# Optimization experiments

Hardware: AMD Instinct MI355X
Metric: run time of the kernel (lower is better)

The kernel has to match this reference:

```python
import jax, jax.numpy as jnp
import numpy as np

EMBED = 1024
HEADS = 16
HEAD_DIM = EMBED // HEADS


def setup_inputs() -> dict:
    key = jax.random.key(0)
    ks = jax.random.split(key, 9)
    N, S = 2, 2048
    values = jax.random.normal(ks[0], (N, S, EMBED), dtype=jnp.float32)
    keys = jax.random.normal(ks[1], (N, S, EMBED), dtype=jnp.float32)
    queries = jax.random.normal(ks[2], (N, S, EMBED), dtype=jnp.float32)
    mask = jax.random.randint(ks[3], (N, 1, S, S), 0, 2, dtype=jnp.int32)
    sc_h = 1.0 / np.sqrt(HEAD_DIM)
    sc_e = 1.0 / np.sqrt(EMBED)
    Wv = jax.random.normal(ks[4], (HEAD_DIM, HEAD_DIM), dtype=jnp.float32) * sc_h
    Wk = jax.random.normal(ks[5], (HEAD_DIM, HEAD_DIM), dtype=jnp.float32) * sc_h
    Wq = jax.random.normal(ks[6], (HEAD_DIM, HEAD_DIM), dtype=jnp.float32) * sc_h
    Wo = jax.random.normal(ks[7], (EMBED, EMBED), dtype=jnp.float32) * sc_e
    bo = jax.random.normal(ks[8], (EMBED,), dtype=jnp.float32) * 0.01
    return {"values": values, "keys": keys, "queries": queries, "mask": mask,
            "Wv": Wv, "Wk": Wk, "Wq": Wq, "Wo": Wo, "bo": bo}


def reference(values, keys, queries, mask, Wv, Wk, Wq, Wo, bo):
    N, S, _ = queries.shape
    H, D = HEADS, HEAD_DIM
    # split heads: [N, S, H, D]
    v = values.reshape(N, -1, H, D) @ Wv.T
    k = keys.reshape(N, -1, H, D) @ Wk.T
    q = queries.reshape(N, -1, H, D) @ Wq.T
    # [N, H, Q, K] scores
    energy = jnp.einsum('nqhd,nkhd->nhqk', q, k)
    energy = jnp.where(mask == 0, jnp.float32(1e-12), energy)
    attention = jax.nn.softmax(energy / np.sqrt(D), axis=3)
    # faithful to source einsum 'NVHD,NHQK->NQHD' (sums V and K independently)
    out = jnp.einsum('nvhd,nhqk->nqhd', v, attention).reshape(N, S, H * D)
    return out @ Wo.T + bo
```

## Files before the change

kernel.cpp:

```cpp
#include <hip/hip_runtime.h>

#define NB     2
#define SEQ    2048
#define EMBED  1024
#define HEADS  16
#define HDIM   64
#define CH     128
#define ROWS   (SEQ / CH)

__global__ __launch_bounds__(256) void colsum_part(const float* __restrict__ vals,
                                                   float* __restrict__ part) {
    const int b = blockIdx.x;
    const int n = b >> 7;
    const int c = b & 127;
    const int t = threadIdx.x;
    const float4* base = reinterpret_cast<const float4*>(vals)
                       + (size_t)(n * SEQ + c * ROWS) * (EMBED / 4);
    float4 acc = make_float4(0.f, 0.f, 0.f, 0.f);
    #pragma unroll 8
    for (int r = 0; r < ROWS; ++r) {
        float4 v = base[(size_t)r * (EMBED / 4) + t];
        acc.x += v.x; acc.y += v.y; acc.z += v.z; acc.w += v.w;
    }
    reinterpret_cast<float4*>(part)[(size_t)b * (EMBED / 4) + t] = acc;
}

__global__ __launch_bounds__(256) void mv_bcast(const float* __restrict__ part,
                                                const float* __restrict__ Wv,
                                                const float* __restrict__ Wo,
                                                const float* __restrict__ bo,
                                                float4* __restrict__ out4) {
    const int b   = blockIdx.x;
    const int wn  = b >> 6;
    const int s16 = b & 63;
    const int t   = threadIdx.x;
    __shared__ float svl[EMBED];
    __shared__ float vfl[EMBED];
    __shared__ float rsl[16];

    {
        const float4* p = reinterpret_cast<const float4*>(part)
                        + (size_t)wn * CH * (EMBED / 4) + t;
        float4 acc = make_float4(0.f, 0.f, 0.f, 0.f);
        #pragma unroll 8
        for (int c = 0; c < CH; ++c) {
            float4 v = p[(size_t)c * (EMBED / 4)];
            acc.x += v.x; acc.y += v.y; acc.z += v.z; acc.w += v.w;
        }
        reinterpret_cast<float4*>(svl)[t] = acc;
    }
    __syncthreads();

    for (int o = t; o < EMBED; o += 256) {
        const int h = o >> 6, d = o & 63;
        const float* wr = Wv + d * HDIM;
        const float* sr = svl + h * HDIM;
        float a = 0.f;
        #pragma unroll
        for (int e = 0; e < HDIM; ++e) a += wr[e] * sr[e];
        vfl[o] = a;
    }
    __syncthreads();

    const int wave = t >> 6;
    const int lane = t & 63;
    float4 vv[4];
    #pragma unroll
    for (int it = 0; it < 4; ++it)
        vv[it] = reinterpret_cast<const float4*>(vfl)[it * 64 + lane];

    const float4* Wo4 = reinterpret_cast<const float4*>(Wo);
    #pragma unroll
    for (int j = 0; j < 4; ++j) {
        const int o = s16 * 16 + wave * 4 + j;
        float acc = 0.f;
        #pragma unroll
        for (int it = 0; it < 4; ++it) {
            float4 w4 = Wo4[(size_t)o * (EMBED / 4) + it * 64 + lane];
            acc += w4.x * vv[it].x + w4.y * vv[it].y
                 + w4.z * vv[it].z + w4.w * vv[it].w;
        }
        #pragma unroll
        for (int off = 32; off >= 1; off >>= 1)
            acc += __shfl_xor(acc, off);
        if (lane == 0) rsl[wave * 4 + j] = acc + bo[o];
    }
    __syncthreads();

    const float4 val = reinterpret_cast<const float4*>(rsl)[t & 3];
    float4* o = out4 + (size_t)wn * SEQ * (EMBED / 4) + (s16 * 4 + (t & 3))
              + (size_t)(t >> 2) * (EMBED / 4);
    #pragma unroll 8
    for (int k = 0; k < 32; ++k)
        o[(size_t)k * 64 * (EMBED / 4)] = val;
}

extern "C" void kernel_launch(void* const* d_in, const int* in_sizes, int n_in,
                              void* d_out, int out_size, void* d_ws, size_t ws_size,
                              hipStream_t stream) {
    const float* vals = (const float*)d_in[0];
    const float* Wv   = (const float*)d_in[4];
    const float* Wo   = (const float*)d_in[7];
    const float* bo   = (const float*)d_in[8];
    float* out = (float*)d_out;

    float* part = (float*)d_ws;

    colsum_part<<<NB * CH, 256, 0, stream>>>(vals, part);
    mv_bcast<<<NB * 64, 256, 0, stream>>>(part, Wv, Wo, bo, (float4*)out);
}
```

Measured before the change: 136.4 us.

## Fuse column-sum and matvec-broadcast into one kernel with global flag sync

Merges the two launches into a single 256-block kernel. Each block first writes its partial column sums and sets a flag. Designated blocks wait on those flags, reduce the partials and publish them with a second set of flags. Every block then waits for the reduced sums and runs the matvec and broadcast. This removes one kernel launch and the gap between the two kernels. In exchange it relies on all blocks being resident at once, and the flags keep the same magic value and are never reset, so on repeated calls the waits may pass early and read stale data.

Result: slower. 169.8 us (+24.5%).

```diff
diff --git a/kernel.cpp b/kernel.cpp
--- a/kernel.cpp
+++ b/kernel.cpp
@@ -3,52 +3,75 @@
 #define NB     2
 #define SEQ    2048
 #define EMBED  1024
-#define HEADS  16
 #define HDIM   64
-#define CH     128
-#define ROWS   (SEQ / CH)
+#define MAGIC  0x3C3C3C3Cu
 
-__global__ __launch_bounds__(256) void colsum_part(const float* __restrict__ vals,
-                                                   float* __restrict__ part) {
+__global__ __launch_bounds__(256) void fused_k(
+    const float* __restrict__ vals, const float* __restrict__ Wv,
+    const float* __restrict__ Wo,  const float* __restrict__ bo,
+    float* __restrict__ part, float* __restrict__ Sv,
+    unsigned* __restrict__ flag1, unsigned* __restrict__ flag2,
+    float4* __restrict__ out4)
+{
     const int b = blockIdx.x;
     const int n = b >> 7;
-    const int c = b & 127;
+    const int j = b & 127;
     const int t = threadIdx.x;
-    const float4* base = reinterpret_cast<const float4*>(vals)
-                       + (size_t)(n * SEQ + c * ROWS) * (EMBED / 4);
-    float4 acc = make_float4(0.f, 0.f, 0.f, 0.f);
-    #pragma unroll 8
-    for (int r = 0; r < ROWS; ++r) {
-        float4 v = base[(size_t)r * (EMBED / 4) + t];
-        acc.x += v.x; acc.y += v.y; acc.z += v.z; acc.w += v.w;
-    }
-    reinterpret_cast<float4*>(part)[(size_t)b * (EMBED / 4) + t] = acc;
-}
 
-__global__ __launch_bounds__(256) void mv_bcast(const float* __restrict__ part,
-                                                const float* __restrict__ Wv,
-                                                const float* __restrict__ Wo,
-                                                const float* __restrict__ bo,
-                                                float4* __restrict__ out4) {
-    const int b   = blockIdx.x;
-    const int wn  = b >> 6;
-    const int s16 = b & 63;
-    const int t   = threadIdx.x;
     __shared__ float svl[EMBED];
     __shared__ float vfl[EMBED];
-    __shared__ float rsl[16];
+    __shared__ float red[256];
+    __shared__ __align__(16) float rsl[16];
 
     {
-        const float4* p = reinterpret_cast<const float4*>(part)
-                        + (size_t)wn * CH * (EMBED / 4) + t;
+        const float4* base = reinterpret_cast<const float4*>(vals)
+                           + (size_t)(n * SEQ + j * 16) * (EMBED / 4);
         float4 acc = make_float4(0.f, 0.f, 0.f, 0.f);
-        #pragma unroll 8
-        for (int c = 0; c < CH; ++c) {
-            float4 v = p[(size_t)c * (EMBED / 4)];
+        #pragma unroll
+        for (int r = 0; r < 16; ++r) {
+            float4 v = base[(size_t)r * (EMBED / 4) + t];
             acc.x += v.x; acc.y += v.y; acc.z += v.z; acc.w += v.w;
         }
-        reinterpret_cast<float4*>(svl)[t] = acc;
+        reinterpret_cast<float4*>(part)[(size_t)b * (EMBED / 4) + t] = acc;
     }
+    __syncthreads();
+    if (t == 0)
+        __hip_atomic_store(&flag1[b], MAGIC, __ATOMIC_RELEASE,
+                           __HIP_MEMORY_SCOPE_AGENT);
+
+    if ((j & 7) == 0) {
+        const int cs = j >> 3;
+        if (t < 128)
+            while (__hip_atomic_load(&flag1[n * 128 + t], __ATOMIC_ACQUIRE,
+                                     __HIP_MEMORY_SCOPE_AGENT) != MAGIC)
+                __builtin_amdgcn_s_sleep(1);
+        __syncthreads();
+        const int i = cs * 64 + (t & 63);
+        const int g = t >> 6;
+        float a = 0.f;
+        #pragma unroll 4
+        for (int c = g; c < 128; c += 4)
+            a += part[(size_t)(n * 128 + c) * EMBED + i];
+        red[t] = a;
+        __syncthreads();
+        if (t < 64)
+            Sv[n * EMBED + cs * 64 + t] =
+                red[t] + red[t + 64] + red[t + 128] + red[t + 192];
+        __syncthreads();
+        if (t == 0)
+            __hip_atomic_store(&flag2[n * 16 + cs], MAGIC, __ATOMIC_RELEASE,
+                               __HIP_MEMORY_SCOPE_AGENT);
+    }
+
+    if (t < 16)
+        while (__hip_atomic_load(&flag2[n * 16 + t], __ATOMIC_ACQUIRE,
+                                 __HIP_MEMORY_SCOPE_AGENT) != MAGIC)
+            __builtin_amdgcn_s_sleep(1);
+    __syncthreads();
+    __threadfence();
+
+    reinterpret_cast<float4*>(svl)[t] =
+        reinterpret_cast<const float4*>(Sv + n * EMBED)[t];
     __syncthreads();
 
     for (int o = t; o < EMBED; o += 256) {
@@ -64,6 +87,8 @@
 
     const int wave = t >> 6;
     const int lane = t & 63;
+    const int s16  = j >> 1;
+    const int hh   = j & 1;
     float4 vv[4];
     #pragma unroll
     for (int it = 0; it < 4; ++it)
@@ -71,8 +96,8 @@
 
     const float4* Wo4 = reinterpret_cast<const float4*>(Wo);
     #pragma unroll
-    for (int j = 0; j < 4; ++j) {
-        const int o = s16 * 16 + wave * 4 + j;
+    for (int j2 = 0; j2 < 4; ++j2) {
+        const int o = s16 * 16 + wave * 4 + j2;
         float acc = 0.f;
         #pragma unroll
         for (int it = 0; it < 4; ++it) {
@@ -83,16 +108,16 @@
         #pragma unroll
         for (int off = 32; off >= 1; off >>= 1)
             acc += __shfl_xor(acc, off);
-        if (lane == 0) rsl[wave * 4 + j] = acc + bo[o];
+        if (lane == 0) rsl[wave * 4 + j2] = acc + bo[o];
     }
     __syncthreads();
 
     const float4 val = reinterpret_cast<const float4*>(rsl)[t & 3];
-    float4* o = out4 + (size_t)wn * SEQ * (EMBED / 4) + (s16 * 4 + (t & 3))
-              + (size_t)(t >> 2) * (EMBED / 4);
-    #pragma unroll 8
-    for (int k = 0; k < 32; ++k)
-        o[(size_t)k * 64 * (EMBED / 4)] = val;
+    float4* op = out4 + (size_t)(n * SEQ + hh * 1024 + (t >> 2)) * (EMBED / 4)
+               + s16 * 4 + (t & 3);
+    #pragma unroll
+    for (int k = 0; k < 16; ++k)
+        op[(size_t)k * 64 * (EMBED / 4)] = val;
 }
 
 extern "C" void kernel_launch(void* const* d_in, const int* in_sizes, int n_in,
@@ -102,10 +127,12 @@
     const float* Wv   = (const float*)d_in[4];
     const float* Wo   = (const float*)d_in[7];
     const float* bo   = (const float*)d_in[8];
-    float* out = (float*)d_out;
 
-    float* part = (float*)d_ws;
+    float*    part  = (float*)d_ws;
+    float*    Sv    = part + (size_t)256 * EMBED;
+    unsigned* flag1 = (unsigned*)(Sv + NB * EMBED);
+    unsigned* flag2 = flag1 + 256;
 
-    colsum_part<<<NB * CH, 256, 0, stream>>>(vals, part);
-    mv_bcast<<<NB * 64, 256, 0, stream>>>(part, Wv, Wo, bo, (float4*)out);
+    fused_k<<<256, 256, 0, stream>>>(vals, Wv, Wo, bo, part, Sv,
+                                     flag1, flag2, (float4*)d_out);
 }
```
